# Performance work log

Measured on AMD Instinct MI355X. Metric: run time of the kernel, lower is better.

The kernel has to match this reference:

```python
import jax, jax.numpy as jnp
import numpy as np

H = 16      # num_heads
D = 64      # nhid (per-head dim)
SL, BS = 1024, 64
DM = 1024   # keys_dim == query_dim == values_dim

def setup_inputs() -> dict:
    key = jax.random.key(0)
    k1, k2, k3, k4, k5 = jax.random.split(key, 5)
    return {
        "query":  jax.random.normal(k1, (BS, DM), dtype=jnp.float32),
        "keys":   jax.random.normal(k2, (SL, BS, DM), dtype=jnp.float32),
        "values": jax.random.normal(k3, (SL, BS, DM), dtype=jnp.float32),
        "Wq":     jax.random.normal(k4, (H * D, DM), dtype=jnp.float32) * 0.02,
        "Wk":     jax.random.normal(k5, (H * D, DM), dtype=jnp.float32) * 0.02,
    }

def reference(query, keys, values, Wq, Wk):
    bs = query.shape[0]
    sl = keys.shape[0]
    scale = jnp.asarray(np.sqrt(D), dtype=query.dtype)
    # projections (note: original module applies keys_linear to values -- a bug we replicate)
    qp = (query @ Wq.T).reshape(bs, H, D)                 # [bs, H, D]
    kp = (keys @ Wk.T).reshape(sl, bs, H, D)              # [sl, bs, H, D]
    vp = (values @ Wk.T).reshape(sl, bs, H, D)            # [sl, bs, H, D]
    # per-head scaled dot-product scores, softmax over the sequence axis (dim 0)
    scores = jnp.einsum('bhd,sbhd->sbh', qp, kp) / scale  # [sl, bs, H]
    attn = jax.nn.softmax(scores, axis=0)
    out = jnp.einsum('sbh,sbhd->bhd', attn, vp)           # [bs, H, D]
    return out.reshape(bs, H * D)
```

## Files before the change

kernel.cpp:

```cpp
#include <hip/hip_runtime.h>
#include <cstddef>
#include <cstdint>

#define NH 16
#define HD 64
#define SLEN 1024
#define NB 64
#define DMODEL 1024

#define DOT4_ACC(acc, k, q) \
  acc = fmaf((k).x, (q).x, fmaf((k).y, (q).y, fmaf((k).z, (q).z, fmaf((k).w, (q).w, (acc)))))

#define FMA4_BCAST(accv, qv, w0_, w1_, w2_, w3_) do { \
  (accv).x = fmaf((qv).x, (w0_).x, fmaf((qv).y, (w1_).x, fmaf((qv).z, (w2_).x, fmaf((qv).w, (w3_).x, (accv).x)))); \
  (accv).y = fmaf((qv).x, (w0_).y, fmaf((qv).y, (w1_).y, fmaf((qv).z, (w2_).y, fmaf((qv).w, (w3_).y, (accv).y)))); \
  (accv).z = fmaf((qv).x, (w0_).z, fmaf((qv).y, (w1_).z, fmaf((qv).z, (w2_).z, fmaf((qv).w, (w3_).z, (accv).z)))); \
  (accv).w = fmaf((qv).x, (w0_).w, fmaf((qv).y, (w1_).w, fmaf((qv).z, (w2_).w, fmaf((qv).w, (w3_).w, (accv).w)))); \
} while (0)

__device__ __forceinline__ float wred_sum(float v) {
#pragma unroll
  for (int off = 32; off; off >>= 1) v += __shfl_xor(v, off, 64);
  return v;
}

__global__ __launch_bounds__(256) void k0_qp(const float* __restrict__ query,
                                             const float* __restrict__ Wq,
                                             float* __restrict__ qp) {
  const int tid = threadIdx.x;
  const int w = tid >> 6, l = tid & 63;
  const int j = blockIdx.x * 4 + w;
  const float4* wr = reinterpret_cast<const float4*>(Wq + (size_t)j * DMODEL) + l * 4;
  const float4 w0 = wr[0], w1 = wr[1], w2 = wr[2], w3 = wr[3];
  for (int b = 0; b < NB; ++b) {
    const float4* qr = reinterpret_cast<const float4*>(query + (size_t)b * DMODEL) + l * 4;
    float4 q0 = qr[0], q1 = qr[1], q2 = qr[2], q3 = qr[3];
    float s = 0.f;
    DOT4_ACC(s, w0, q0); DOT4_ACC(s, w1, q1); DOT4_ACC(s, w2, q2); DOT4_ACC(s, w3, q3);
    s = wred_sum(s);
    if (l == 0) qp[(size_t)b * DMODEL + j] = s;
  }
}

__global__ __launch_bounds__(256) void k1_qt(const float* __restrict__ qp,
                                             const float* __restrict__ Wk,
                                             float* __restrict__ qt) {
  __shared__ __align__(16) float qpl[8][HD];
  const int h = blockIdx.x & 15;
  const int b0 = (blockIdx.x >> 4) * 8;
  const int tid = threadIdx.x;
  for (int f = tid; f < 8 * HD; f += 256) {
    int bi = f >> 6, d = f & 63;
    qpl[bi][d] = qp[(size_t)(b0 + bi) * DMODEL + h * HD + d];
  }
  __syncthreads();
  const int m4 = tid * 4;
  float4 acc[8];
#pragma unroll
  for (int i = 0; i < 8; ++i) acc[i] = make_float4(0.f, 0.f, 0.f, 0.f);
  const float* wbase = Wk + (size_t)(h * HD) * DMODEL + m4;
  for (int d = 0; d < HD; d += 4) {
    float4 wk0 = *reinterpret_cast<const float4*>(wbase + (size_t)(d + 0) * DMODEL);
    float4 wk1 = *reinterpret_cast<const float4*>(wbase + (size_t)(d + 1) * DMODEL);
    float4 wk2 = *reinterpret_cast<const float4*>(wbase + (size_t)(d + 2) * DMODEL);
    float4 wk3 = *reinterpret_cast<const float4*>(wbase + (size_t)(d + 3) * DMODEL);
#pragma unroll
    for (int bi = 0; bi < 8; ++bi) {
      float4 q = *reinterpret_cast<const float4*>(&qpl[bi][d]);
      FMA4_BCAST(acc[bi], q, wk0, wk1, wk2, wk3);
    }
  }
#pragma unroll
  for (int bi = 0; bi < 8; ++bi)
    *reinterpret_cast<float4*>(qt + ((size_t)(b0 + bi) * NH + h) * DMODEL + m4) = acc[bi];
}

__global__ __launch_bounds__(128) void k2_scores(const float* __restrict__ keys,
                                                 const float* __restrict__ qt,
                                                 float* __restrict__ scp) {
  __shared__ __align__(16) float ql[NH][512];
  const int b  = blockIdx.x & 63;
  const int st = (blockIdx.x >> 6) & 7;
  const int mh = blockIdx.x >> 9;
  const int tid = threadIdx.x, w = tid >> 6, l = tid & 63;
  const int hg = l & 3;
  const int sg = l >> 2;
  for (int f = tid; f < 2048; f += 128) {
    int hh = f >> 7, m4 = (f & 127) * 4;
    *reinterpret_cast<float4*>(&ql[hh][m4]) = *reinterpret_cast<const float4*>(
        qt + ((size_t)b * NH + hh) * DMODEL + mh * 512 + m4);
  }
  __syncthreads();
  const int s_base = st * 128 + w * 64 + sg;
  const float* kp0 = keys + ((size_t)(s_base +  0) * NB + b) * DMODEL + mh * 512 + hg * 4;
  const float* kp1 = keys + ((size_t)(s_base + 16) * NB + b) * DMODEL + mh * 512 + hg * 4;
  const float* kp2 = keys + ((size_t)(s_base + 32) * NB + b) * DMODEL + mh * 512 + hg * 4;
  const float* kp3 = keys + ((size_t)(s_base + 48) * NB + b) * DMODEL + mh * 512 + hg * 4;
  float acc[4][NH];
#pragma unroll
  for (int si = 0; si < 4; ++si)
#pragma unroll
    for (int hh = 0; hh < NH; ++hh) acc[si][hh] = 0.f;
#pragma unroll 4
  for (int m = 0; m < 512; m += 16) {
    float4 k0 = *reinterpret_cast<const float4*>(kp0 + m);
    float4 k1 = *reinterpret_cast<const float4*>(kp1 + m);
    float4 k2 = *reinterpret_cast<const float4*>(kp2 + m);
    float4 k3 = *reinterpret_cast<const float4*>(kp3 + m);
#pragma unroll
    for (int hh = 0; hh < NH; ++hh) {
      float4 q = *reinterpret_cast<const float4*>(&ql[hh][m + hg * 4]);
      DOT4_ACC(acc[0][hh], k0, q);
      DOT4_ACC(acc[1][hh], k1, q);
      DOT4_ACC(acc[2][hh], k2, q);
      DOT4_ACC(acc[3][hh], k3, q);
    }
  }
#pragma unroll
  for (int si = 0; si < 4; ++si)
#pragma unroll
    for (int hh = 0; hh < NH; ++hh) {
      acc[si][hh] += __shfl_xor(acc[si][hh], 1, 64);
      acc[si][hh] += __shfl_xor(acc[si][hh], 2, 64);
    }
  const float scale = 0.125f;
  float* plane = scp + (size_t)mh * NB * NH * SLEN;
#pragma unroll
  for (int j = 0; j < 4; ++j) {
    float* o = plane + ((size_t)b * NH + hg * 4 + j) * SLEN + s_base;
#pragma unroll
    for (int si = 0; si < 4; ++si) {
      float r = hg == 0 ? acc[si][j] : hg == 1 ? acc[si][4 + j]
              : hg == 2 ? acc[si][8 + j] : acc[si][12 + j];
      o[si * 16] = r * scale;
    }
  }
}

__global__ __launch_bounds__(256) void k_sm(float* __restrict__ sc0,
                                            const float* __restrict__ sc1) {
  __shared__ float red[8];
  const int tid = threadIdx.x, w = tid >> 6, l = tid & 63;
  float* p0 = sc0 + (size_t)blockIdx.x * SLEN;
  const float* p1 = sc1 + (size_t)blockIdx.x * SLEN;
  float4 xa = reinterpret_cast<const float4*>(p0)[tid];
  float4 xb = reinterpret_cast<const float4*>(p1)[tid];
  float4 x = make_float4(xa.x + xb.x, xa.y + xb.y, xa.z + xb.z, xa.w + xb.w);
  float mx = fmaxf(fmaxf(x.x, x.y), fmaxf(x.z, x.w));
#pragma unroll
  for (int off = 32; off; off >>= 1) mx = fmaxf(mx, __shfl_xor(mx, off, 64));
  if (l == 0) red[w] = mx;
  __syncthreads();
  mx = fmaxf(fmaxf(red[0], red[1]), fmaxf(red[2], red[3]));
  float4 e;
  e.x = __expf(x.x - mx); e.y = __expf(x.y - mx);
  e.z = __expf(x.z - mx); e.w = __expf(x.w - mx);
  float sum = e.x + e.y + e.z + e.w;
  sum = wred_sum(sum);
  if (l == 0) red[4 + w] = sum;
  __syncthreads();
  sum = red[4] + red[5] + red[6] + red[7];
  const float inv = 1.f / sum;
  e.x *= inv; e.y *= inv; e.z *= inv; e.w *= inv;
  reinterpret_cast<float4*>(p0)[tid] = e;
}

template <int NCH>
__global__ __launch_bounds__(256) void k3_cpart(const float* __restrict__ values,
                                                const float* __restrict__ attn,
                                                float* __restrict__ cp) {
  constexpr int SC = SLEN / NCH;
  __shared__ __align__(16) float al[NH * SC];
  const int b = blockIdx.x & 63;
  const int ch = blockIdx.x >> 6;
  const int s0 = ch * SC;
  const int tid = threadIdx.x;
  for (int f = tid; f < NH * SC / 4; f += 256) {
    int hh = f / (SC / 4), c4 = f % (SC / 4);
    *reinterpret_cast<float4*>(&al[hh * SC + c4 * 4]) =
        *reinterpret_cast<const float4*>(attn + ((size_t)b * NH + hh) * SLEN + s0 + c4 * 4);
  }
  __syncthreads();
  const int m4 = tid * 4;
  float4 acc[NH];
#pragma unroll
  for (int i = 0; i < NH; ++i) acc[i] = make_float4(0.f, 0.f, 0.f, 0.f);
  const float* vbase = values + ((size_t)s0 * NB + b) * DMODEL + m4;
#pragma unroll 2
  for (int sl = 0; sl < SC; sl += 4) {
    const float* vp = vbase + (size_t)sl * NB * DMODEL;
    float4 v0 = *reinterpret_cast<const float4*>(vp);
    float4 v1 = *reinterpret_cast<const float4*>(vp + (size_t)1 * NB * DMODEL);
    float4 v2 = *reinterpret_cast<const float4*>(vp + (size_t)2 * NB * DMODEL);
    float4 v3 = *reinterpret_cast<const float4*>(vp + (size_t)3 * NB * DMODEL);
#pragma unroll
    for (int hh = 0; hh < NH; ++hh) {
      float4 a = *reinterpret_cast<const float4*>(&al[hh * SC + sl]);
      FMA4_BCAST(acc[hh], a, v0, v1, v2, v3);
    }
  }
#pragma unroll
  for (int hh = 0; hh < NH; ++hh)
    *reinterpret_cast<float4*>(cp + (((size_t)ch * NB + b) * NH + hh) * DMODEL + m4) = acc[hh];
}

template <int NCH>
__global__ __launch_bounds__(256) void k4_out(const float* __restrict__ cp,
                                              const float* __restrict__ Wk,
                                              float* __restrict__ out) {
  __shared__ __align__(16) float cl[4 * DMODEL];
  const int h = blockIdx.x & 15;
  const int b0 = (blockIdx.x >> 4) * 4;
  const int tid = threadIdx.x, w = tid >> 6, l = tid & 63;
  for (int f = tid; f < 4 * DMODEL / 4; f += 256) {
    int bi = f >> 8, m4 = (f & 255) * 4;
    float4 s = make_float4(0.f, 0.f, 0.f, 0.f);
#pragma unroll
    for (int ch = 0; ch < NCH; ++ch) {
      float4 t = *reinterpret_cast<const float4*>(
          cp + (((size_t)ch * NB + b0 + bi) * NH + h) * DMODEL + m4);
      s.x += t.x; s.y += t.y; s.z += t.z; s.w += t.w;
    }
    *reinterpret_cast<float4*>(&cl[bi * DMODEL + m4]) = s;
  }
  __syncthreads();
  float4 c[4][4];
#pragma unroll
  for (int bi = 0; bi < 4; ++bi)
#pragma unroll
    for (int k = 0; k < 4; ++k)
      c[bi][k] = *reinterpret_cast<const float4*>(&cl[bi * DMODEL + l * 16 + k * 4]);
  for (int jj = 0; jj < 16; ++jj) {
    const int d = w * 16 + jj;
    const float4* wr = reinterpret_cast<const float4*>(Wk + (size_t)(h * HD + d) * DMODEL) + l * 4;
    const float4 w0 = wr[0], w1 = wr[1], w2 = wr[2], w3 = wr[3];
#pragma unroll
    for (int bi = 0; bi < 4; ++bi) {
      float s = 0.f;
      DOT4_ACC(s, w0, c[bi][0]); DOT4_ACC(s, w1, c[bi][1]);
      DOT4_ACC(s, w2, c[bi][2]); DOT4_ACC(s, w3, c[bi][3]);
      s = wred_sum(s);
      if (l == 0) out[(size_t)(b0 + bi) * (NH * HD) + h * HD + d] = s;
    }
  }
}

extern "C" void kernel_launch(void* const* d_in, const int* in_sizes, int n_in,
                              void* d_out, int out_size, void* d_ws, size_t ws_size,
                              hipStream_t stream) {
  const float* query  = (const float*)d_in[0];
  const float* keys   = (const float*)d_in[1];
  const float* values = (const float*)d_in[2];
  const float* Wq     = (const float*)d_in[3];
  const float* Wk     = (const float*)d_in[4];
  float* out = (float*)d_out;

  float* W   = (float*)d_ws;
  float* qp  = W;
  float* qt  = qp + (size_t)NB * DMODEL;
  float* sc0 = qt + (size_t)NB * NH * DMODEL;
  float* sc1 = sc0 + (size_t)NB * NH * SLEN;
  float* cp  = sc1 + (size_t)NB * NH * SLEN;

  const size_t base_floats = (size_t)NB * DMODEL + (size_t)NB * NH * DMODEL
                           + 2 * (size_t)NB * NH * SLEN;

  k0_qp<<<256, 256, 0, stream>>>(query, Wq, qp);
  k1_qt<<<128, 256, 0, stream>>>(qp, Wk, qt);
  k2_scores<<<1024, 128, 0, stream>>>(keys, qt, sc0);
  k_sm<<<NB * NH, 256, 0, stream>>>(sc0, sc1);

  const size_t chunk_floats = (size_t)NB * NH * DMODEL;
  if (ws_size >= (base_floats + 16 * chunk_floats) * sizeof(float)) {
    k3_cpart<16><<<16 * NB, 256, 0, stream>>>(values, sc0, cp);
    k4_out<16><<<NH * (NB / 4), 256, 0, stream>>>(cp, Wk, out);
  } else if (ws_size >= (base_floats + 8 * chunk_floats) * sizeof(float)) {
    k3_cpart<8><<<8 * NB, 256, 0, stream>>>(values, sc0, cp);
    k4_out<8><<<NH * (NB / 4), 256, 0, stream>>>(cp, Wk, out);
  } else if (ws_size >= (base_floats + 4 * chunk_floats) * sizeof(float)) {
    k3_cpart<4><<<4 * NB, 256, 0, stream>>>(values, sc0, cp);
    k4_out<4><<<NH * (NB / 4), 256, 0, stream>>>(cp, Wk, out);
  } else {
    k3_cpart<2><<<2 * NB, 256, 0, stream>>>(values, sc0, cp);
    k4_out<2><<<NH * (NB / 4), 256, 0, stream>>>(cp, Wk, out);
  }
}
```

Measured before the change: 255.0 us.

## Stage keys and values tiles into LDS via global_load_lds in scores and context kernels

The scores and context-partial kernels now load key and value rows with direct global-to-LDS async loads into shared tiles, with an XOR swizzle for keys, instead of per-thread global float4 loads. Threads then read their operands from LDS. This aims to improve coalescing and cut VGPR pressure from global loads. In exchange it adds two block barriers per chunk and single-buffered staging with no prefetch, which can expose memory latency. The smallest-workspace NCH=2 fallback path is removed.

```diff
diff --git a/kernel.cpp b/kernel.cpp
--- a/kernel.cpp
+++ b/kernel.cpp
@@ -22,6 +22,12 @@
 #pragma unroll
   for (int off = 32; off; off >>= 1) v += __shfl_xor(v, off, 64);
   return v;
+}
+
+__device__ __forceinline__ void gload16(const float* g, float* lds_base) {
+  __builtin_amdgcn_global_load_lds(
+      (const __attribute__((address_space(1))) void*)g,
+      (__attribute__((address_space(3))) void*)lds_base, 16, 0, 0);
 }
 
 __global__ __launch_bounds__(256) void k0_qp(const float* __restrict__ query,
@@ -79,42 +85,54 @@
                                                  const float* __restrict__ qt,
                                                  float* __restrict__ scp) {
   __shared__ __align__(16) float ql[NH][512];
+  __shared__ __align__(16) float kb[128 * 16];
   const int b  = blockIdx.x & 63;
   const int st = (blockIdx.x >> 6) & 7;
   const int mh = blockIdx.x >> 9;
   const int tid = threadIdx.x, w = tid >> 6, l = tid & 63;
   const int hg = l & 3;
   const int sg = l >> 2;
-  for (int f = tid; f < 2048; f += 128) {
+  for (int f = tid; f < NH * 128; f += 128) {
     int hh = f >> 7, m4 = (f & 127) * 4;
     *reinterpret_cast<float4*>(&ql[hh][m4]) = *reinterpret_cast<const float4*>(
         qt + ((size_t)b * NH + hh) * DMODEL + mh * 512 + m4);
   }
-  __syncthreads();
-  const int s_base = st * 128 + w * 64 + sg;
-  const float* kp0 = keys + ((size_t)(s_base +  0) * NB + b) * DMODEL + mh * 512 + hg * 4;
-  const float* kp1 = keys + ((size_t)(s_base + 16) * NB + b) * DMODEL + mh * 512 + hg * 4;
-  const float* kp2 = keys + ((size_t)(s_base + 32) * NB + b) * DMODEL + mh * 512 + hg * 4;
-  const float* kp3 = keys + ((size_t)(s_base + 48) * NB + b) * DMODEL + mh * 512 + hg * 4;
+  const int s0 = st * 128;
+  const size_t rowstride = (size_t)NB * DMODEL;
+  const float* kbase = keys + ((size_t)s0 * NB + b) * DMODEL + mh * 512;
+  const int srow  = l >> 2;
+  const int sslot = (l & 3) ^ (srow & 3);
   float acc[4][NH];
 #pragma unroll
   for (int si = 0; si < 4; ++si)
 #pragma unroll
     for (int hh = 0; hh < NH; ++hh) acc[si][hh] = 0.f;
-#pragma unroll 4
-  for (int m = 0; m < 512; m += 16) {
-    float4 k0 = *reinterpret_cast<const float4*>(kp0 + m);
-    float4 k1 = *reinterpret_cast<const float4*>(kp1 + m);
-    float4 k2 = *reinterpret_cast<const float4*>(kp2 + m);
-    float4 k3 = *reinterpret_cast<const float4*>(kp3 + m);
+  const int sl0 = w * 64 + sg;
+
+  for (int ch = 0; ch < 32; ++ch) {
+#pragma unroll
+    for (int i = 0; i < 4; ++i) {
+      const int u = w * 4 + i;
+      const int row = u * 16 + srow;
+      const float* g = kbase + (size_t)row * rowstride + ch * 16 + sslot * 4;
+      gload16(g, &kb[u * 256]);
+    }
+    __syncthreads();
+    float4 kv[4];
+#pragma unroll
+    for (int si = 0; si < 4; ++si) {
+      const int s = sl0 + si * 16;
+      kv[si] = *reinterpret_cast<const float4*>(&kb[s * 16 + ((hg ^ (s & 3)) << 2)]);
+    }
 #pragma unroll
     for (int hh = 0; hh < NH; ++hh) {
-      float4 q = *reinterpret_cast<const float4*>(&ql[hh][m + hg * 4]);
-      DOT4_ACC(acc[0][hh], k0, q);
-      DOT4_ACC(acc[1][hh], k1, q);
-      DOT4_ACC(acc[2][hh], k2, q);
-      DOT4_ACC(acc[3][hh], k3, q);
-    }
+      float4 q = *reinterpret_cast<const float4*>(&ql[hh][ch * 16 + hg * 4]);
+      DOT4_ACC(acc[0][hh], kv[0], q);
+      DOT4_ACC(acc[1][hh], kv[1], q);
+      DOT4_ACC(acc[2][hh], kv[2], q);
+      DOT4_ACC(acc[3][hh], kv[3], q);
+    }
+    __syncthreads();
   }
 #pragma unroll
   for (int si = 0; si < 4; ++si)
@@ -127,12 +145,11 @@
   float* plane = scp + (size_t)mh * NB * NH * SLEN;
 #pragma unroll
   for (int j = 0; j < 4; ++j) {
-    float* o = plane + ((size_t)b * NH + hg * 4 + j) * SLEN + s_base;
 #pragma unroll
     for (int si = 0; si < 4; ++si) {
       float r = hg == 0 ? acc[si][j] : hg == 1 ? acc[si][4 + j]
               : hg == 2 ? acc[si][8 + j] : acc[si][12 + j];
-      o[si * 16] = r * scale;
+      plane[((size_t)b * NH + hg * 4 + j) * SLEN + s0 + sl0 + si * 16] = r * scale;
     }
   }
 }
@@ -170,34 +187,42 @@
                                                 const float* __restrict__ attn,
                                                 float* __restrict__ cp) {
   constexpr int SC = SLEN / NCH;
-  __shared__ __align__(16) float al[NH * SC];
+  __shared__ __align__(16) float vb[4][DMODEL];
+  __shared__ __align__(16) float al[NH][SC];
   const int b = blockIdx.x & 63;
   const int ch = blockIdx.x >> 6;
   const int s0 = ch * SC;
-  const int tid = threadIdx.x;
-  for (int f = tid; f < NH * SC / 4; f += 256) {
-    int hh = f / (SC / 4), c4 = f % (SC / 4);
-    *reinterpret_cast<float4*>(&al[hh * SC + c4 * 4]) =
-        *reinterpret_cast<const float4*>(attn + ((size_t)b * NH + hh) * SLEN + s0 + c4 * 4);
-  }
-  __syncthreads();
+  const int tid = threadIdx.x, w = tid >> 6, l = tid & 63;
+  for (int f = tid; f < NH * (SC / 4); f += 256) {
+    int hh = f / (SC / 4), c4 = (f % (SC / 4)) * 4;
+    *reinterpret_cast<float4*>(&al[hh][c4]) = *reinterpret_cast<const float4*>(
+        attn + ((size_t)b * NH + hh) * SLEN + s0 + c4);
+  }
   const int m4 = tid * 4;
   float4 acc[NH];
 #pragma unroll
   for (int i = 0; i < NH; ++i) acc[i] = make_float4(0.f, 0.f, 0.f, 0.f);
-  const float* vbase = values + ((size_t)s0 * NB + b) * DMODEL + m4;
-#pragma unroll 2
-  for (int sl = 0; sl < SC; sl += 4) {
-    const float* vp = vbase + (size_t)sl * NB * DMODEL;
-    float4 v0 = *reinterpret_cast<const float4*>(vp);
-    float4 v1 = *reinterpret_cast<const float4*>(vp + (size_t)1 * NB * DMODEL);
-    float4 v2 = *reinterpret_cast<const float4*>(vp + (size_t)2 * NB * DMODEL);
-    float4 v3 = *reinterpret_cast<const float4*>(vp + (size_t)3 * NB * DMODEL);
+  const size_t rowstride = (size_t)NB * DMODEL;
+  const float* vbase = values + ((size_t)s0 * NB + b) * DMODEL;
+
+  for (int g = 0; g < SC / 4; ++g) {
+    {
+      const float* rg = vbase + (size_t)(g * 4 + w) * rowstride;
+#pragma unroll
+      for (int j = 0; j < 4; ++j)
+        gload16(rg + j * 256 + l * 4, &vb[w][j * 256]);
+    }
+    __syncthreads();
+    float4 v0 = *reinterpret_cast<const float4*>(&vb[0][m4]);
+    float4 v1 = *reinterpret_cast<const float4*>(&vb[1][m4]);
+    float4 v2 = *reinterpret_cast<const float4*>(&vb[2][m4]);
+    float4 v3 = *reinterpret_cast<const float4*>(&vb[3][m4]);
 #pragma unroll
     for (int hh = 0; hh < NH; ++hh) {
-      float4 a = *reinterpret_cast<const float4*>(&al[hh * SC + sl]);
-      FMA4_BCAST(acc[hh], a, v0, v1, v2, v3);
-    }
+      float4 av = *reinterpret_cast<const float4*>(&al[hh][g * 4]);
+      FMA4_BCAST(acc[hh], av, v0, v1, v2, v3);
+    }
+    __syncthreads();
   }
 #pragma unroll
   for (int hh = 0; hh < NH; ++hh)
@@ -277,11 +302,8 @@
   } else if (ws_size >= (base_floats + 8 * chunk_floats) * sizeof(float)) {
     k3_cpart<8><<<8 * NB, 256, 0, stream>>>(values, sc0, cp);
     k4_out<8><<<NH * (NB / 4), 256, 0, stream>>>(cp, Wk, out);
-  } else if (ws_size >= (base_floats + 4 * chunk_floats) * sizeof(float)) {
+  } else {
     k3_cpart<4><<<4 * NB, 256, 0, stream>>>(values, sc0, cp);
     k4_out<4><<<NH * (NB / 4), 256, 0, stream>>>(cp, Wk, out);
-  } else {
-    k3_cpart<2><<<2 * NB, 256, 0, stream>>>(values, sc0, cp);
-    k4_out<2><<<NH * (NB / 4), 256, 0, stream>>>(cp, Wk, out);
-  }
-}
+  }
+}
```

Result: no change. 255.4 us (+0.2%).
